# Performance work log

Measured on AMD Instinct MI355X. Metric: run time of the kernel, lower is better.

## Reference

```python
import jax, jax.numpy as jnp
import numpy as np

B, H, L, D = 4, 16, 2048, 64


def setup_inputs() -> dict:
    key = jax.random.key(0)
    k1, k2, k3 = jax.random.split(key, 3)
    return {
        "query": jax.random.normal(k1, (B, H, L, D), dtype=jnp.float32),
        "key": jax.random.normal(k2, (B, H, L, D), dtype=jnp.float32),
        "value": jax.random.normal(k3, (B, H, D, L), dtype=jnp.float32),
    }


def reference(query, key, value):
    # dot_product_score = Q @ K^T / sqrt(D)   -> [B,H,L,L]
    d = query.shape[-1]
    scores = jnp.einsum("bhqd,bhkd->bhqk", query, key) / jnp.sqrt(jnp.asarray(d, query.dtype))
    attn = jax.nn.softmax(scores, axis=-1)
    # NOTE: original module returns matmul(value, attention_score) = V @ A
    # (value contracted over its last dim L with attn's query dim L) -> [B,H,D,L]
    return jnp.matmul(value, attn)
```

## Files before the change

kernel.cpp:

```cpp
#include <hip/hip_runtime.h>
#include <hip/hip_bf16.h>

#define L_SEQ 2048
#define D_HEAD 64
#define NHEADS 64
#define QSCALE (0.125f * 1.44269504088896340736f)

typedef __attribute__((ext_vector_type(8))) __bf16 bf16x8;
typedef __attribute__((ext_vector_type(16))) float f32x16;

__device__ __forceinline__ int swz(int row, int col) {
    int off = (row << 7) | (col << 1);
    return off ^ ((row & 7) << 4);
}
__device__ __forceinline__ bf16x8 read_frag(const char* lds, int row, int col) {
    return *reinterpret_cast<const bf16x8*>(lds + swz(row, col));
}
__device__ __forceinline__ void pack_write(char* lds, int row, int c4, float4 v,
                                           float4 sc) {
    union { __bf16 h[4]; unsigned long long u; } pk;
    pk.h[0] = (__bf16)(v.x * sc.x);
    pk.h[1] = (__bf16)(v.y * sc.y);
    pk.h[2] = (__bf16)(v.z * sc.z);
    pk.h[3] = (__bf16)(v.w * sc.w);
    *reinterpret_cast<unsigned long long*>(lds + swz(row, c4)) = pk.u;
}

__device__ __forceinline__ unsigned cvt_pk_bf16(float lo, float hi) {
    unsigned r;
    asm("v_cvt_pk_bf16_f32 %0, %1, %2" : "=v"(r) : "v"(lo), "v"(hi));
    return r;
}

__global__ __launch_bounds__(256, 4) void attn_pass1(const float* __restrict__ Q,
                                                     const float* __restrict__ K,
                                                     float* __restrict__ invl) {
    __shared__ __align__(16) char lds[16384];
    __shared__ float red[2][128];

    int bid = blockIdx.x;
    int sb = (bid & 7) * 128 + (bid >> 3);
    int bh = sb >> 4;
    int q0 = (sb & 15) << 7;
    const float* Qh = Q + (size_t)bh * L_SEQ * D_HEAD + (size_t)q0 * D_HEAD;
    const float* Kh = K + (size_t)bh * L_SEQ * D_HEAD;

    int t = threadIdx.x, lane = t & 63, w = t >> 6;
    int wq = w >> 1, wk = w & 1;
    int hl = lane >> 5, l31 = lane & 31;
    int r0 = t >> 4;
    int c4 = (t & 15) << 2;

    {
        float4 qs = make_float4(QSCALE, QSCALE, QSCALE, QSCALE);
#pragma unroll
        for (int i = 0; i < 8; ++i) {
            float4 v = *reinterpret_cast<const float4*>(Qh + (size_t)(r0 + i * 16) * D_HEAD + c4);
            pack_write(lds, r0 + i * 16, c4, v, qs);
        }
    }
    __syncthreads();
    bf16x8 qfrag[2][4];
#pragma unroll
    for (int qb = 0; qb < 2; ++qb)
#pragma unroll
        for (int m = 0; m < 4; ++m)
            qfrag[qb][m] = read_frag(lds, wq * 64 + qb * 32 + l31, m * 16 + hl * 8);
    __syncthreads();
    {
        float4 one = make_float4(1.f, 1.f, 1.f, 1.f);
#pragma unroll
        for (int i = 0; i < 4; ++i) {
            float4 v = *reinterpret_cast<const float4*>(Kh + (size_t)(r0 + i * 16) * D_HEAD + c4);
            pack_write(lds, r0 + i * 16, c4, v, one);
        }
    }
    __syncthreads();

    float lsum[2][16];
#pragma unroll
    for (int qb = 0; qb < 2; ++qb)
#pragma unroll
        for (int r = 0; r < 16; ++r) lsum[qb][r] = 0.f;

    for (int k0 = 0; k0 < L_SEQ; k0 += 64) {
        int c = (k0 >> 6) & 1;
        const char* kcur = lds + (c ? 8192 : 0);
        char* knext = lds + (c ? 0 : 8192);

        int nk0 = (k0 + 64) & (L_SEQ - 1);
        float4 kreg[4];
#pragma unroll
        for (int i = 0; i < 4; ++i)
            kreg[i] = *reinterpret_cast<const float4*>(Kh + (size_t)(nk0 + r0 + i * 16) * D_HEAD + c4);

        bf16x8 kfr[4];
#pragma unroll
        for (int m = 0; m < 4; ++m)
            kfr[m] = read_frag(kcur, wk * 32 + l31, m * 16 + hl * 8);

        __builtin_amdgcn_s_setprio(1);
#pragma unroll
        for (int qb = 0; qb < 2; ++qb) {
            f32x16 s;
#pragma unroll
            for (int r = 0; r < 16; ++r) s[r] = 0.f;
#pragma unroll
            for (int m = 0; m < 4; ++m)
                s = __builtin_amdgcn_mfma_f32_32x32x16_bf16(qfrag[qb][m], kfr[m], s, 0, 0, 0);
#pragma unroll
            for (int r = 0; r < 16; ++r)
                lsum[qb][r] += __builtin_amdgcn_exp2f(s[r]);
        }
        __builtin_amdgcn_s_setprio(0);

        {
            float4 one = make_float4(1.f, 1.f, 1.f, 1.f);
#pragma unroll
            for (int i = 0; i < 4; ++i)
                pack_write(knext, r0 + i * 16, c4, kreg[i], one);
        }
        __syncthreads();
    }

#pragma unroll
    for (int qb = 0; qb < 2; ++qb)
#pragma unroll
        for (int r = 0; r < 16; ++r) {
            float v = lsum[qb][r];
            v += __shfl_xor(v, 1);
            v += __shfl_xor(v, 2);
            v += __shfl_xor(v, 4);
            v += __shfl_xor(v, 8);
            v += __shfl_xor(v, 16);
            lsum[qb][r] = v;
        }
    if (l31 == 0) {
#pragma unroll
        for (int qb = 0; qb < 2; ++qb)
#pragma unroll
            for (int r = 0; r < 16; ++r)
                red[wk][wq * 64 + qb * 32 + (r & 3) + 8 * (r >> 2) + 4 * hl] = lsum[qb][r];
    }
    __syncthreads();
    if (t < 128) {
        float ssum = red[0][t] + red[1][t];
        invl[(size_t)bh * L_SEQ + q0 + t] = 1.0f / ssum;
    }
}

__global__ __launch_bounds__(256, 2) void attn_pass2(const float* __restrict__ Q,
                                                     const float* __restrict__ K,
                                                     const float* __restrict__ V,
                                                     const float* __restrict__ invl,
                                                     float* __restrict__ out) {
    __shared__ __align__(16) char lds[65536];

    int bid = blockIdx.x;
    int sb = (bid & 7) * 64 + (bid >> 3);
    int bh = sb >> 3;
    int k0 = (sb & 7) << 8;
    const float* Qh = Q + (size_t)bh * L_SEQ * D_HEAD;
    const float* Kh = K + (size_t)bh * L_SEQ * D_HEAD + (size_t)k0 * D_HEAD;
    const float* Vh = V + (size_t)bh * D_HEAD * L_SEQ;
    const float* il = invl + (size_t)bh * L_SEQ;
    float* Oh = out + (size_t)bh * D_HEAD * L_SEQ;

    int t = threadIdx.x, lane = t & 63, w = t >> 6;
    int hl = lane >> 5, l31 = lane & 31;
    int r0 = t >> 4;
    int c4 = (t & 15) << 2;

    {
        float4 one = make_float4(1.f, 1.f, 1.f, 1.f);
#pragma unroll
        for (int i = 0; i < 16; i += 4) {
            float4 kr[4];
#pragma unroll
            for (int j = 0; j < 4; ++j)
                kr[j] = *reinterpret_cast<const float4*>(Kh + (size_t)(r0 + (i + j) * 16) * D_HEAD + c4);
#pragma unroll
            for (int j = 0; j < 4; ++j)
                pack_write(lds, r0 + (i + j) * 16, c4, kr[j], one);
        }
    }
    __syncthreads();
    bf16x8 kfrag[2][4];
#pragma unroll
    for (int kb = 0; kb < 2; ++kb)
#pragma unroll
        for (int m = 0; m < 4; ++m)
            kfrag[kb][m] = read_frag(lds, w * 64 + kb * 32 + l31, m * 16 + hl * 8);

    {
        float4 qs = make_float4(QSCALE, QSCALE, QSCALE, QSCALE);
        float4 iv = *reinterpret_cast<const float4*>(il + c4);
#pragma unroll
        for (int i = 0; i < 4; ++i) {
            float4 qv = *reinterpret_cast<const float4*>(Qh + (size_t)(r0 + i * 16) * D_HEAD + c4);
            float4 vv = *reinterpret_cast<const float4*>(Vh + (size_t)(r0 + i * 16) * L_SEQ + c4);
            pack_write(lds + 32768, r0 + i * 16, c4, qv, qs);
            pack_write(lds + 49152, r0 + i * 16, c4, vv, iv);
        }
    }
    __syncthreads();

    f32x16 acc[2][2];
#pragma unroll
    for (int db = 0; db < 2; ++db)
#pragma unroll
        for (int kb = 0; kb < 2; ++kb)
#pragma unroll
            for (int r = 0; r < 16; ++r) acc[db][kb][r] = 0.f;

    for (int q0 = 0; q0 < L_SEQ; q0 += 64) {
        int c = (q0 >> 6) & 1;
        const char* qcur = lds + 32768 + (c ? 8192 : 0);
        const char* vcur = lds + 49152 + (c ? 8192 : 0);
        char* qnext = lds + 32768 + (c ? 0 : 8192);
        char* vnext = lds + 49152 + (c ? 0 : 8192);

        int nq0 = (q0 + 64) & (L_SEQ - 1);
        float4 qreg[4], vreg[4];
#pragma unroll
        for (int i = 0; i < 4; ++i) {
            qreg[i] = *reinterpret_cast<const float4*>(Qh + (size_t)(nq0 + r0 + i * 16) * D_HEAD + c4);
            vreg[i] = *reinterpret_cast<const float4*>(Vh + (size_t)(r0 + i * 16) * L_SEQ + nq0 + c4);
        }
        float4 ivn = *reinterpret_cast<const float4*>(il + nq0 + c4);

#pragma unroll
        for (int qq = 0; qq < 2; ++qq) {
            f32x16 s[2];
#pragma unroll
            for (int kb = 0; kb < 2; ++kb)
#pragma unroll
                for (int r = 0; r < 16; ++r) s[kb][r] = 0.f;

            __builtin_amdgcn_s_setprio(1);
#pragma unroll
            for (int m = 0; m < 4; ++m) {
                bf16x8 afr = read_frag(qcur, qq * 32 + l31, m * 16 + hl * 8);
                s[0] = __builtin_amdgcn_mfma_f32_32x32x16_bf16(afr, kfrag[0][m], s[0], 0, 0, 0);
                s[1] = __builtin_amdgcn_mfma_f32_32x32x16_bf16(afr, kfrag[1][m], s[1], 0, 0, 0);
            }
            __builtin_amdgcn_s_setprio(0);

            bf16x8 pfrag[2][2];
#pragma unroll
            for (int kb = 0; kb < 2; ++kb) {
                unsigned wA[4], wB[4];
#pragma unroll
                for (int g = 0; g < 4; ++g) {
                    wA[g] = cvt_pk_bf16(__builtin_amdgcn_exp2f(s[kb][4 * g + 0]),
                                        __builtin_amdgcn_exp2f(s[kb][4 * g + 1]));
                    wB[g] = cvt_pk_bf16(__builtin_amdgcn_exp2f(s[kb][4 * g + 2]),
                                        __builtin_amdgcn_exp2f(s[kb][4 * g + 3]));
                }
#pragma unroll
                for (int mm = 0; mm < 2; ++mm) {
                    unsigned a0 = wA[2 * mm], b0 = wA[2 * mm + 1];
                    unsigned a1 = wB[2 * mm], b1 = wB[2 * mm + 1];
                    asm volatile("v_permlane32_swap_b32 %0, %1" : "+v"(a0), "+v"(b0));
                    asm volatile("v_permlane32_swap_b32 %0, %1" : "+v"(a1), "+v"(b1));
                    union { unsigned u[4]; bf16x8 v; } pk;
                    pk.u[0] = a0;
                    pk.u[1] = a1;
                    pk.u[2] = b0;
                    pk.u[3] = b1;
                    pfrag[kb][mm] = pk.v;
                }
            }

            __builtin_amdgcn_s_setprio(1);
#pragma unroll
            for (int mm = 0; mm < 2; ++mm)
#pragma unroll
                for (int db = 0; db < 2; ++db) {
                    bf16x8 vfr = read_frag(vcur, db * 32 + l31, qq * 32 + mm * 16 + hl * 8);
#pragma unroll
                    for (int kb = 0; kb < 2; ++kb)
                        acc[db][kb] = __builtin_amdgcn_mfma_f32_32x32x16_bf16(
                            vfr, pfrag[kb][mm], acc[db][kb], 0, 0, 0);
                }
            __builtin_amdgcn_s_setprio(0);
        }

        {
            float4 qs = make_float4(QSCALE, QSCALE, QSCALE, QSCALE);
#pragma unroll
            for (int i = 0; i < 4; ++i) {
                pack_write(qnext, r0 + i * 16, c4, qreg[i], qs);
                pack_write(vnext, r0 + i * 16, c4, vreg[i], ivn);
            }
        }
        __syncthreads();
    }

#pragma unroll
    for (int db = 0; db < 2; ++db)
#pragma unroll
        for (int kb = 0; kb < 2; ++kb)
#pragma unroll
            for (int r = 0; r < 16; ++r) {
                int d = db * 32 + (r & 3) + 8 * (r >> 2) + 4 * hl;
                int k = k0 + w * 64 + kb * 32 + l31;
                Oh[(size_t)d * L_SEQ + k] = acc[db][kb][r];
            }
}

extern "C" void kernel_launch(void* const* d_in, const int* in_sizes, int n_in,
                              void* d_out, int out_size, void* d_ws, size_t ws_size,
                              hipStream_t stream) {
    const float* Q = (const float*)d_in[0];
    const float* K = (const float*)d_in[1];
    const float* V = (const float*)d_in[2];
    float* invl = (float*)d_ws;
    float* out = (float*)d_out;

    attn_pass1<<<dim3(NHEADS * (L_SEQ / 128)), dim3(256), 0, stream>>>(Q, K, invl);
    attn_pass2<<<dim3(NHEADS * (L_SEQ / 256)), dim3(256), 0, stream>>>(Q, K, V, invl, out);
}
```

Before: 142.5 us.

## Split pass2 query dimension across wave pairs with LDS reduction of partial outputs

Pass 2 now gives each block 128 key columns instead of 256, so twice as many blocks are launched. The four waves form a 2x2 grid: two key halves, and two query halves of each 64-query tile. Each wave accumulates a partial V·P, and the two query-half partials are summed through LDS at the end. LDS drops to 32KB and launch bounds allow 4 blocks per CU to raise occupancy, at the cost of Q/V tile loads being amortised over half as many keys and an extra reduction step.

New measurement: 349.7 us. 2.45x slower.

```diff
diff --git a/kernel.cpp b/kernel.cpp
--- a/kernel.cpp
+++ b/kernel.cpp
@@ -149,17 +149,17 @@
     }
 }
 
-__global__ __launch_bounds__(256, 2) void attn_pass2(const float* __restrict__ Q,
+__global__ __launch_bounds__(256, 4) void attn_pass2(const float* __restrict__ Q,
                                                      const float* __restrict__ K,
                                                      const float* __restrict__ V,
                                                      const float* __restrict__ invl,
                                                      float* __restrict__ out) {
-    __shared__ __align__(16) char lds[65536];
+    __shared__ __align__(16) char lds[32768];
 
     int bid = blockIdx.x;
-    int sb = (bid & 7) * 64 + (bid >> 3);
-    int bh = sb >> 3;
-    int k0 = (sb & 7) << 8;
+    int sb = (bid & 7) * 128 + (bid >> 3);
+    int bh = sb >> 4;
+    int k0 = (sb & 15) << 7;
     const float* Qh = Q + (size_t)bh * L_SEQ * D_HEAD;
     const float* Kh = K + (size_t)bh * L_SEQ * D_HEAD + (size_t)k0 * D_HEAD;
     const float* Vh = V + (size_t)bh * D_HEAD * L_SEQ;
@@ -167,6 +167,7 @@
     float* Oh = out + (size_t)bh * D_HEAD * L_SEQ;
 
     int t = threadIdx.x, lane = t & 63, w = t >> 6;
+    int wq = w >> 1, wk = w & 1;
     int hl = lane >> 5, l31 = lane & 31;
     int r0 = t >> 4;
     int c4 = (t & 15) << 2;
@@ -174,14 +175,9 @@
     {
         float4 one = make_float4(1.f, 1.f, 1.f, 1.f);
 #pragma unroll
-        for (int i = 0; i < 16; i += 4) {
-            float4 kr[4];
-#pragma unroll
-            for (int j = 0; j < 4; ++j)
-                kr[j] = *reinterpret_cast<const float4*>(Kh + (size_t)(r0 + (i + j) * 16) * D_HEAD + c4);
-#pragma unroll
-            for (int j = 0; j < 4; ++j)
-                pack_write(lds, r0 + (i + j) * 16, c4, kr[j], one);
+        for (int i = 0; i < 8; ++i) {
+            float4 v = *reinterpret_cast<const float4*>(Kh + (size_t)(r0 + i * 16) * D_HEAD + c4);
+            pack_write(lds, r0 + i * 16, c4, v, one);
         }
     }
     __syncthreads();
@@ -190,7 +186,7 @@
     for (int kb = 0; kb < 2; ++kb)
 #pragma unroll
         for (int m = 0; m < 4; ++m)
-            kfrag[kb][m] = read_frag(lds, w * 64 + kb * 32 + l31, m * 16 + hl * 8);
+            kfrag[kb][m] = read_frag(lds, wk * 64 + kb * 32 + l31, m * 16 + hl * 8);
 
     {
         float4 qs = make_float4(QSCALE, QSCALE, QSCALE, QSCALE);
@@ -199,8 +195,8 @@
         for (int i = 0; i < 4; ++i) {
             float4 qv = *reinterpret_cast<const float4*>(Qh + (size_t)(r0 + i * 16) * D_HEAD + c4);
             float4 vv = *reinterpret_cast<const float4*>(Vh + (size_t)(r0 + i * 16) * L_SEQ + c4);
-            pack_write(lds + 32768, r0 + i * 16, c4, qv, qs);
-            pack_write(lds + 49152, r0 + i * 16, c4, vv, iv);
+            pack_write(lds + 16384, r0 + i * 16, c4, qv, qs);
+            pack_write(lds + 24576, r0 + i * 16, c4, vv, iv);
         }
     }
     __syncthreads();
@@ -215,10 +211,10 @@
 
     for (int q0 = 0; q0 < L_SEQ; q0 += 64) {
         int c = (q0 >> 6) & 1;
-        const char* qcur = lds + 32768 + (c ? 8192 : 0);
-        const char* vcur = lds + 49152 + (c ? 8192 : 0);
-        char* qnext = lds + 32768 + (c ? 0 : 8192);
-        char* vnext = lds + 49152 + (c ? 0 : 8192);
+        const char* qcur = lds + (c ? 0 : 16384);
+        const char* vcur = lds + (c ? 8192 : 24576);
+        char* qnext = lds + (c ? 16384 : 0);
+        char* vnext = lds + (c ? 24576 : 8192);
 
         int nq0 = (q0 + 64) & (L_SEQ - 1);
         float4 qreg[4], vreg[4];
@@ -229,62 +225,59 @@
         }
         float4 ivn = *reinterpret_cast<const float4*>(il + nq0 + c4);
 
-#pragma unroll
-        for (int qq = 0; qq < 2; ++qq) {
-            f32x16 s[2];
-#pragma unroll
-            for (int kb = 0; kb < 2; ++kb)
-#pragma unroll
-                for (int r = 0; r < 16; ++r) s[kb][r] = 0.f;
-
-            __builtin_amdgcn_s_setprio(1);
-#pragma unroll
-            for (int m = 0; m < 4; ++m) {
-                bf16x8 afr = read_frag(qcur, qq * 32 + l31, m * 16 + hl * 8);
-                s[0] = __builtin_amdgcn_mfma_f32_32x32x16_bf16(afr, kfrag[0][m], s[0], 0, 0, 0);
-                s[1] = __builtin_amdgcn_mfma_f32_32x32x16_bf16(afr, kfrag[1][m], s[1], 0, 0, 0);
+        f32x16 s[2];
+#pragma unroll
+        for (int kb = 0; kb < 2; ++kb)
+#pragma unroll
+            for (int r = 0; r < 16; ++r) s[kb][r] = 0.f;
+
+        __builtin_amdgcn_s_setprio(1);
+#pragma unroll
+        for (int m = 0; m < 4; ++m) {
+            bf16x8 afr = read_frag(qcur, wq * 32 + l31, m * 16 + hl * 8);
+            s[0] = __builtin_amdgcn_mfma_f32_32x32x16_bf16(afr, kfrag[0][m], s[0], 0, 0, 0);
+            s[1] = __builtin_amdgcn_mfma_f32_32x32x16_bf16(afr, kfrag[1][m], s[1], 0, 0, 0);
+        }
+        __builtin_amdgcn_s_setprio(0);
+
+        bf16x8 pfrag[2][2];
+#pragma unroll
+        for (int kb = 0; kb < 2; ++kb) {
+            unsigned wA[4], wB[4];
+#pragma unroll
+            for (int g = 0; g < 4; ++g) {
+                wA[g] = cvt_pk_bf16(__builtin_amdgcn_exp2f(s[kb][4 * g + 0]),
+                                    __builtin_amdgcn_exp2f(s[kb][4 * g + 1]));
+                wB[g] = cvt_pk_bf16(__builtin_amdgcn_exp2f(s[kb][4 * g + 2]),
+                                    __builtin_amdgcn_exp2f(s[kb][4 * g + 3]));
             }
-            __builtin_amdgcn_s_setprio(0);
-
-            bf16x8 pfrag[2][2];
-#pragma unroll
-            for (int kb = 0; kb < 2; ++kb) {
-                unsigned wA[4], wB[4];
-#pragma unroll
-                for (int g = 0; g < 4; ++g) {
-                    wA[g] = cvt_pk_bf16(__builtin_amdgcn_exp2f(s[kb][4 * g + 0]),
-                                        __builtin_amdgcn_exp2f(s[kb][4 * g + 1]));
-                    wB[g] = cvt_pk_bf16(__builtin_amdgcn_exp2f(s[kb][4 * g + 2]),
-                                        __builtin_amdgcn_exp2f(s[kb][4 * g + 3]));
-                }
-#pragma unroll
-                for (int mm = 0; mm < 2; ++mm) {
-                    unsigned a0 = wA[2 * mm], b0 = wA[2 * mm + 1];
-                    unsigned a1 = wB[2 * mm], b1 = wB[2 * mm + 1];
-                    asm volatile("v_permlane32_swap_b32 %0, %1" : "+v"(a0), "+v"(b0));
-                    asm volatile("v_permlane32_swap_b32 %0, %1" : "+v"(a1), "+v"(b1));
-                    union { unsigned u[4]; bf16x8 v; } pk;
-                    pk.u[0] = a0;
-                    pk.u[1] = a1;
-                    pk.u[2] = b0;
-                    pk.u[3] = b1;
-                    pfrag[kb][mm] = pk.v;
-                }
+#pragma unroll
+            for (int mm = 0; mm < 2; ++mm) {
+                unsigned a0 = wA[2 * mm], b0 = wA[2 * mm + 1];
+                unsigned a1 = wB[2 * mm], b1 = wB[2 * mm + 1];
+                asm volatile("v_permlane32_swap_b32 %0, %1" : "+v"(a0), "+v"(b0));
+                asm volatile("v_permlane32_swap_b32 %0, %1" : "+v"(a1), "+v"(b1));
+                union { unsigned u[4]; bf16x8 v; } pk;
+                pk.u[0] = a0;
+                pk.u[1] = a1;
+                pk.u[2] = b0;
+                pk.u[3] = b1;
+                pfrag[kb][mm] = pk.v;
             }
-
-            __builtin_amdgcn_s_setprio(1);
-#pragma unroll
-            for (int mm = 0; mm < 2; ++mm)
-#pragma unroll
-                for (int db = 0; db < 2; ++db) {
-                    bf16x8 vfr = read_frag(vcur, db * 32 + l31, qq * 32 + mm * 16 + hl * 8);
-#pragma unroll
-                    for (int kb = 0; kb < 2; ++kb)
-                        acc[db][kb] = __builtin_amdgcn_mfma_f32_32x32x16_bf16(
-                            vfr, pfrag[kb][mm], acc[db][kb], 0, 0, 0);
-                }
-            __builtin_amdgcn_s_setprio(0);
-        }
+        }
+
+        __builtin_amdgcn_s_setprio(1);
+#pragma unroll
+        for (int mm = 0; mm < 2; ++mm)
+#pragma unroll
+            for (int db = 0; db < 2; ++db) {
+                bf16x8 vfr = read_frag(vcur, db * 32 + l31, wq * 32 + mm * 16 + hl * 8);
+#pragma unroll
+                for (int kb = 0; kb < 2; ++kb)
+                    acc[db][kb] = __builtin_amdgcn_mfma_f32_32x32x16_bf16(
+                        vfr, pfrag[kb][mm], acc[db][kb], 0, 0, 0);
+            }
+        __builtin_amdgcn_s_setprio(0);
 
         {
             float4 qs = make_float4(QSCALE, QSCALE, QSCALE, QSCALE);
@@ -297,16 +290,32 @@
         __syncthreads();
     }
 
-#pragma unroll
-    for (int db = 0; db < 2; ++db)
-#pragma unroll
-        for (int kb = 0; kb < 2; ++kb)
-#pragma unroll
-            for (int r = 0; r < 16; ++r) {
-                int d = db * 32 + (r & 3) + 8 * (r >> 2) + 4 * hl;
-                int k = k0 + w * 64 + kb * 32 + l31;
-                Oh[(size_t)d * L_SEQ + k] = acc[db][kb][r];
-            }
+    __syncthreads();
+    float* exf = reinterpret_cast<float*>(lds);
+    if (wq == 1) {
+#pragma unroll
+        for (int db = 0; db < 2; ++db)
+#pragma unroll
+            for (int kb = 0; kb < 2; ++kb)
+#pragma unroll
+                for (int r = 0; r < 16; ++r)
+                    exf[(((wk * 2 + db) * 2 + kb) * 16 + r) * 64 + lane] = acc[db][kb][r];
+    }
+    __syncthreads();
+    if (wq == 0) {
+#pragma unroll
+        for (int db = 0; db < 2; ++db)
+#pragma unroll
+            for (int kb = 0; kb < 2; ++kb)
+#pragma unroll
+                for (int r = 0; r < 16; ++r) {
+                    float v = acc[db][kb][r] +
+                              exf[(((wk * 2 + db) * 2 + kb) * 16 + r) * 64 + lane];
+                    int d = db * 32 + (r & 3) + 8 * (r >> 2) + 4 * hl;
+                    int k = k0 + wk * 64 + kb * 32 + l31;
+                    Oh[(size_t)d * L_SEQ + k] = v;
+                }
+    }
 }
 
 extern "C" void kernel_launch(void* const* d_in, const int* in_sizes, int n_in,
@@ -319,5 +328,5 @@
     float* out = (float*)d_out;
 
     attn_pass1<<<dim3(NHEADS * (L_SEQ / 128)), dim3(256), 0, stream>>>(Q, K, invl);
-    attn_pass2<<<dim3(NHEADS * (L_SEQ / 256)), dim3(256), 0, stream>>>(Q, K, V, invl, out);
-}
+    attn_pass2<<<dim3(NHEADS * (L_SEQ / 128)), dim3(256), 0, stream>>>(Q, K, V, invl, out);
+}
```
